# Performance work log

Measured on AMD Instinct MI355X. Metric: run time of the kernel, lower is better.

## Reference

```python
import jax, jax.numpy as jnp
import numpy as np

N_NODES, N_EDGES = 50000, 800000
IN_DIM, OUT_DIM, EDGE_DIM = 128, 128, 32
NUM_HEADS = 8
HEAD_DIM = OUT_DIM // NUM_HEADS
SCALE = HEAD_DIM ** -0.5


def setup_inputs() -> dict:
    key = jax.random.key(0)
    ks = jax.random.split(key, 8)
    def lin_w(k, fan_in, fan_out):
        # kaiming-uniform-ish init like nn.Linear
        bound = 1.0 / np.sqrt(fan_in)
        return jax.random.uniform(k, (fan_in, fan_out), jnp.float32, -bound, bound)
    return {
        "node_features": jax.random.normal(ks[0], (N_NODES, IN_DIM), jnp.float32),
        "edge_features": jax.random.normal(ks[1], (N_EDGES, EDGE_DIM), jnp.float32),
        "Wq": lin_w(ks[2], IN_DIM, OUT_DIM), "bq": jnp.zeros((OUT_DIM,), jnp.float32),
        "Wk": lin_w(ks[3], IN_DIM, OUT_DIM), "bk": jnp.zeros((OUT_DIM,), jnp.float32),
        "Wv": lin_w(ks[4], IN_DIM, OUT_DIM), "bv": jnp.zeros((OUT_DIM,), jnp.float32),
        "We": lin_w(ks[5], EDGE_DIM, OUT_DIM), "be": jnp.zeros((OUT_DIM,), jnp.float32),
        "edge_list": jax.random.randint(ks[6], (N_EDGES, 2), 0, N_NODES, jnp.int32),
        "num_nodes": N_NODES,
    }


def reference(node_features, edge_features, Wq, bq, Wk, bk, Wv, bv, We, be, edge_list, num_nodes):
    # node projections -> [N, H, D]
    Q = (node_features @ Wq + bq).reshape(-1, NUM_HEADS, HEAD_DIM)
    K = (node_features @ Wk + bk).reshape(-1, NUM_HEADS, HEAD_DIM)
    V = (node_features @ Wv + bv).reshape(-1, NUM_HEADS, HEAD_DIM)
    edge_bias = (edge_features @ We + be).reshape(-1, NUM_HEADS, HEAD_DIM)

    src = edge_list[:, 0]  # node_in
    dst = edge_list[:, 1]  # node_out

    # per-edge per-head scores: [E, H]
    scores = jnp.einsum("ehd,ehd->eh", Q[src], K[dst]) * SCALE + edge_bias.sum(-1)
    # NOTE: softmax over the HEADS axis (dim=1), exactly as in the source
    weights = jax.nn.softmax(scores, axis=1)

    # weighted messages gathered from src, scattered to dst: [E, H, D] -> [N, H, D]
    msg = V[src] * weights[..., None]
    node_updates = jax.ops.segment_sum(msg, dst, num_segments=num_nodes)
    return node_updates.reshape(num_nodes, OUT_DIM)
```

## Files before the change

kernel.cpp:

```cpp
#include <hip/hip_runtime.h>
#include <math.h>

#define IN_DIM   128
#define OUT_DIM  128
#define EDGE_DIM 32
#define NUM_HEADS 8
#define HEAD_DIM 16
#define SCALE 0.25f
#define CSTRIDE 16

typedef __attribute__((ext_vector_type(8))) short bf16x8;
typedef __attribute__((ext_vector_type(4))) float f32x4;
typedef __attribute__((ext_vector_type(4))) unsigned int u32x4;

__device__ inline unsigned short f2bf(float x) {
    unsigned int u = __float_as_uint(x);
    unsigned int r = u + 0x7fff + ((u >> 16) & 1);
    return (unsigned short)(r >> 16);
}
__device__ inline float bflo(unsigned int u) { return __uint_as_float(u << 16); }
__device__ inline float bfhi(unsigned int u) { return __uint_as_float(u & 0xffff0000u); }

__global__ __launch_bounds__(256) void setup_kernel(
    int* __restrict__ counts, int n_nodes, int nbz,
    const float* __restrict__ Wq, const float* __restrict__ Wk,
    const float* __restrict__ Wv, unsigned short* __restrict__ WtB, int nbw,
    const float* __restrict__ We, const float* __restrict__ be,
    float* __restrict__ WeR, float* __restrict__ beR,
    const float* __restrict__ X, unsigned short* __restrict__ Xb)
{
    const int bx = blockIdx.x;
    const int t  = threadIdx.x;
    if (bx < nbz) {
        const int i = bx * 256 + t;
        if (i < n_nodes) counts[i << 4] = 0;
    } else if (bx < nbz + nbw) {
        const int idx = (bx - nbz) * 256 + t;
        const int mat = idx >> 14;
        const int rem = idx & 16383;
        const int n = rem >> 7, k = rem & 127;
        const float* W = (mat == 0) ? Wq : (mat == 1) ? Wk : Wv;
        WtB[mat * 16384 + n * 128 + k] = f2bf(W[k * 128 + n]);
    } else if (bx == nbz + nbw) {
        const int k = t >> 3, h = t & 7;
        float s = 0.f;
#pragma unroll
        for (int d = 0; d < HEAD_DIM; ++d) s += We[k * OUT_DIM + h * HEAD_DIM + d];
        WeR[k * NUM_HEADS + h] = s;
        if (t < NUM_HEADS) {
            float sb = 0.f;
#pragma unroll
            for (int d = 0; d < HEAD_DIM; ++d) sb += be[t * HEAD_DIM + d];
            beR[t] = sb;
        }
    } else {
        const int i = (bx - (nbz + nbw + 1)) * 256 + t;
        if (i < n_nodes * 16) {
            const f32x4* xr = (const f32x4*)(X + (size_t)i * 8);
            const f32x4 x0 = xr[0], x1 = xr[1];
            u32x4 p;
            p[0] = (unsigned)f2bf(x0[0]) | ((unsigned)f2bf(x0[1]) << 16);
            p[1] = (unsigned)f2bf(x0[2]) | ((unsigned)f2bf(x0[3]) << 16);
            p[2] = (unsigned)f2bf(x1[0]) | ((unsigned)f2bf(x1[1]) << 16);
            p[3] = (unsigned)f2bf(x1[2]) | ((unsigned)f2bf(x1[3]) << 16);
            *(u32x4*)(Xb + (size_t)i * 8) = p;
        }
    }
}

__global__ __launch_bounds__(256) void edge_kernel(
    const int* __restrict__ el, int* __restrict__ counts, int* __restrict__ rank,
    const float* __restrict__ ef, const float* __restrict__ WeR,
    const float* __restrict__ beR, unsigned int* __restrict__ ebias_e,
    int n_edges)
{
    const int e = blockIdx.x * 256 + threadIdx.x;
    if (e >= n_edges) return;
    const int2 ed = ((const int2*)el)[e];
    rank[e] = atomicAdd(&counts[ed.y << 4], 1);

    float acc[NUM_HEADS];
#pragma unroll
    for (int h = 0; h < NUM_HEADS; ++h) acc[h] = beR[h];

    const f32x4* efr = (const f32x4*)(ef + (size_t)e * EDGE_DIM);
#pragma unroll
    for (int kk = 0; kk < 8; ++kk) {
        const f32x4 f = efr[kk];
#pragma unroll
        for (int c = 0; c < 4; ++c) {
            const float* wr = WeR + (kk * 4 + c) * NUM_HEADS;
#pragma unroll
            for (int h = 0; h < NUM_HEADS; ++h)
                acc[h] = fmaf(f[c], wr[h], acc[h]);
        }
    }
    u32x4 pk;
    pk[0] = (unsigned)f2bf(acc[0]) | ((unsigned)f2bf(acc[1]) << 16);
    pk[1] = (unsigned)f2bf(acc[2]) | ((unsigned)f2bf(acc[3]) << 16);
    pk[2] = (unsigned)f2bf(acc[4]) | ((unsigned)f2bf(acc[5]) << 16);
    pk[3] = (unsigned)f2bf(acc[6]) | ((unsigned)f2bf(acc[7]) << 16);
    *(u32x4*)(ebias_e + (size_t)e * 4) = pk;
}

__global__ __launch_bounds__(256) void qkv_kernel(
    const unsigned short* __restrict__ Xb, const unsigned short* __restrict__ WtB,
    const float* __restrict__ bq, const float* __restrict__ bk,
    const float* __restrict__ bv,
    unsigned short* __restrict__ QVb, unsigned short* __restrict__ Kb,
    int n_nodes, int nbm)
{
    __shared__ unsigned short shW[16384];
    const int bx = blockIdx.x;
    const int t  = threadIdx.x;

    const int which = bx / nbm;
    const int mb    = bx - which * nbm;
    const unsigned short* Wg = WtB + which * 16384;

#pragma unroll
    for (int kk = 0; kk < 8; ++kk) {
        const int c = kk * 256 + t;
        const u32x4 v = ((const u32x4*)Wg)[c];
        const int row = c >> 4;
        const int bir = (c & 15) << 4;
        *(u32x4*)((char*)shW + row * 256 + (bir ^ ((row & 7) << 4))) = v;
    }
    __syncthreads();

    const int wave = t >> 6, lane = t & 63;
    const int quad = lane >> 4, li = lane & 15;
    const int mbase = mb * 256 + wave * 64;

    int mrow[4];
#pragma unroll
    for (int m = 0; m < 4; ++m) {
        const int r_ = mbase + m * 16 + li;
        mrow[m] = (r_ < n_nodes) ? r_ : (n_nodes - 1);
    }

    f32x4 acc[4][8];
#pragma unroll
    for (int m = 0; m < 4; ++m)
#pragma unroll
        for (int nt = 0; nt < 8; ++nt) acc[m][nt] = (f32x4){0.f, 0.f, 0.f, 0.f};

#pragma unroll
    for (int ks = 0; ks < 4; ++ks) {
        bf16x8 a[4];
#pragma unroll
        for (int m = 0; m < 4; ++m)
            a[m] = *(const bf16x8*)(Xb + (size_t)mrow[m] * 128 + ks * 32 + quad * 8);
#pragma unroll
        for (int nt = 0; nt < 8; ++nt) {
            const int row = nt * 16 + li;
            const bf16x8 b = *(const bf16x8*)((const char*)shW + row * 256 +
                                ((ks * 64 + quad * 16) ^ ((row & 7) << 4)));
#pragma unroll
            for (int m = 0; m < 4; ++m)
                acc[m][nt] = __builtin_amdgcn_mfma_f32_16x16x32_bf16(a[m], b, acc[m][nt], 0, 0, 0);
        }
    }

    const float* bias = (which == 0) ? bq : (which == 1) ? bk : bv;
    float bv8[8];
#pragma unroll
    for (int nt = 0; nt < 8; ++nt) bv8[nt] = bias[nt * 16 + li];

    __syncthreads();

    unsigned short* stg = shW + wave * 2176;
    const int R = lane >> 2, cc4 = lane & 3;
#pragma unroll
    for (int m = 0; m < 4; ++m) {
#pragma unroll
        for (int nt = 0; nt < 8; ++nt)
#pragma unroll
            for (int r = 0; r < 4; ++r)
                stg[(quad * 4 + r) * 136 + nt * 16 + li] = f2bf(acc[m][nt][r] + bv8[nt]);
        __syncthreads();

        const int node = mbase + m * 16 + R;
        if (node < n_nodes) {
            const u32x4* s = (const u32x4*)(stg + R * 136 + cc4 * 32);
            u32x4 d0 = s[0], d1 = s[1], d2 = s[2], d3 = s[3];
            unsigned short* dp =
                (which == 0) ? (QVb + (size_t)node * 256 + cc4 * 32)
              : (which == 1) ? (Kb  + (size_t)node * 128 + cc4 * 32)
              :                (QVb + (size_t)node * 256 + 128 + cc4 * 32);
            u32x4* d = (u32x4*)dp;
            d[0] = d0; d[1] = d1; d[2] = d2; d[3] = d3;
        }
        __syncthreads();
    }
}

__global__ __launch_bounds__(256) void scan1_kernel(
    const int* __restrict__ counts, int* __restrict__ bsums, int n)
{
    __shared__ int lds[256];
    const int i = blockIdx.x * 256 + threadIdx.x;
    lds[threadIdx.x] = (i < n) ? counts[i << 4] : 0;
    __syncthreads();
    for (int off = 128; off > 0; off >>= 1) {
        if (threadIdx.x < off) lds[threadIdx.x] += lds[threadIdx.x + off];
        __syncthreads();
    }
    if (threadIdx.x == 0) bsums[blockIdx.x] = lds[0];
}

__global__ __launch_bounds__(256) void scan3_kernel(
    const int* __restrict__ counts, const int* __restrict__ bsums,
    int* __restrict__ offsets, int n, int n_edges, int nb)
{
    __shared__ int lds[256];
    const int t = threadIdx.x;

    int v = (t < nb) ? bsums[t] : 0;
    lds[t] = v;
    __syncthreads();
    for (int off = 1; off < 256; off <<= 1) {
        const int u = (t >= off) ? lds[t - off] : 0;
        __syncthreads();
        lds[t] += u;
        __syncthreads();
    }
    const int base = (blockIdx.x > 0) ? lds[blockIdx.x - 1] : 0;
    __syncthreads();

    const int i = blockIdx.x * 256 + t;
    const int c = (i < n) ? counts[i << 4] : 0;
    lds[t] = c;
    __syncthreads();
    for (int off = 1; off < 256; off <<= 1) {
        const int u = (t >= off) ? lds[t - off] : 0;
        __syncthreads();
        lds[t] += u;
        __syncthreads();
    }
    if (i < n) offsets[i] = base + lds[t] - c;
    if (blockIdx.x == 0 && t == 0) offsets[n] = n_edges;
}

__global__ __launch_bounds__(256) void scatter_kernel(
    const int* __restrict__ el, const int* __restrict__ rank,
    const unsigned int* __restrict__ ebias_e,
    const int* __restrict__ offsets, unsigned int* __restrict__ recs,
    int n_edges)
{
    const int e = blockIdx.x * 256 + threadIdx.x;
    if (e >= n_edges) return;
    const int2 ed = ((const int2*)el)[e];
    const u32x4 eb = *(const u32x4*)(ebias_e + (size_t)e * 4);
    const int pos = offsets[ed.y] + rank[e];

    u32x4 r0, r1;
    r0[0] = (unsigned)ed.x;
    r0[1] = 0;
    r0[2] = eb[0];
    r0[3] = eb[1];
    r1[0] = eb[2];
    r1[1] = eb[3];
    r1[2] = 0; r1[3] = 0;
    u32x4* rp = (u32x4*)(recs + (size_t)pos * 8);
    rp[0] = r0;
    rp[1] = r1;
}

__global__ __launch_bounds__(256) void aggregate_kernel(
    const unsigned short* __restrict__ QVb, const unsigned short* __restrict__ Kb,
    const int* __restrict__ offsets, const unsigned int* __restrict__ recs,
    float* __restrict__ out, int n_nodes)
{
    const int gw   = (blockIdx.x * 256 + threadIdx.x) >> 6;
    const int lane = threadIdx.x & 63;
    const int half = lane >> 5, ln = lane & 31;
    const int node = gw * 2 + half;
    const int h = ln >> 2;
    const bool valid = node < n_nodes;

    int beg = 0, end = 0;
    if (valid) { beg = offsets[node]; end = offsets[node + 1]; }
    const int cnt = end - beg;
    const int mcnt = max(cnt, __shfl_xor(cnt, 32));

    float k0 = 0.f, k1 = 0.f, k2 = 0.f, k3 = 0.f;
    if (valid) {
        const uint2 kp = ((const uint2*)(Kb + (size_t)node * 128))[ln];
        k0 = bflo(kp.x); k1 = bfhi(kp.x); k2 = bflo(kp.y); k3 = bfhi(kp.y);
    }

    float a0 = 0.f, a1 = 0.f, a2 = 0.f, a3 = 0.f;

    uint2 qp = make_uint2(0, 0), vp = make_uint2(0, 0);
    float eb = 0.f;
    if (cnt > 0) {
        const unsigned int* rb = recs + (size_t)beg * 8;
        const int src = (int)rb[0];
        const unsigned int ebp = rb[2 + (h >> 1)];
        eb = (h & 1) ? bfhi(ebp) : bflo(ebp);
        const uint2* r = (const uint2*)(QVb + (size_t)src * 256);
        qp = r[ln];
        vp = r[32 + ln];
    }

    for (int i = 0; i < mcnt; ++i) {
        uint2 nqp = qp, nvp = vp;
        float neb = eb;
        if (i + 1 < cnt) {
            const unsigned int* rb = recs + (size_t)(beg + i + 1) * 8;
            const int ns = (int)rb[0];
            const unsigned int ebp = rb[2 + (h >> 1)];
            neb = (h & 1) ? bfhi(ebp) : bflo(ebp);
            const uint2* r = (const uint2*)(QVb + (size_t)ns * 256);
            nqp = r[ln];
            nvp = r[32 + ln];
        }

        const float q0 = bflo(qp.x), q1 = bfhi(qp.x);
        const float q2 = bflo(qp.y), q3 = bfhi(qp.y);
        float p = fmaf(q0, k0, fmaf(q1, k1, fmaf(q2, k2, q3 * k3)));
        p += __shfl_xor(p, 1);
        p += __shfl_xor(p, 2);
        const float score = fmaf(p, SCALE, eb);

        float mx = score;
        mx = fmaxf(mx, __shfl_xor(mx, 4));
        mx = fmaxf(mx, __shfl_xor(mx, 8));
        mx = fmaxf(mx, __shfl_xor(mx, 16));
        const float ex = __expf(score - mx);
        float den = ex;
        den += __shfl_xor(den, 4);
        den += __shfl_xor(den, 8);
        den += __shfl_xor(den, 16);
        const float w = __fdividef(ex, den);

        if (i < cnt) {
            a0 = fmaf(w, bflo(vp.x), a0);
            a1 = fmaf(w, bfhi(vp.x), a1);
            a2 = fmaf(w, bflo(vp.y), a2);
            a3 = fmaf(w, bfhi(vp.y), a3);
        }
        qp = nqp; vp = nvp; eb = neb;
    }

    if (valid) {
        f32x4 o; o[0] = a0; o[1] = a1; o[2] = a2; o[3] = a3;
        *(((f32x4*)(out + (size_t)node * OUT_DIM)) + ln) = o;
    }
}

extern "C" void kernel_launch(void* const* d_in, const int* in_sizes, int n_in,
                              void* d_out, int out_size, void* d_ws, size_t ws_size,
                              hipStream_t stream)
{
    const float* X   = (const float*)d_in[0];
    const float* ef  = (const float*)d_in[1];
    const float* Wq  = (const float*)d_in[2];
    const float* bq  = (const float*)d_in[3];
    const float* Wk  = (const float*)d_in[4];
    const float* bk  = (const float*)d_in[5];
    const float* Wv  = (const float*)d_in[6];
    const float* bv  = (const float*)d_in[7];
    const float* We  = (const float*)d_in[8];
    const float* be  = (const float*)d_in[9];
    const int*   el  = (const int*)d_in[10];

    const int n_nodes = in_sizes[0] / IN_DIM;
    const int n_edges = in_sizes[10] / 2;

    char* w = (char*)d_ws;
    auto alloc = [&](size_t bytes) { char* p = w; w += (bytes + 255) & ~(size_t)255; return p; };

    unsigned short* QVb    = (unsigned short*)alloc((size_t)n_nodes * 256 * 2);
    unsigned short* Kb     = (unsigned short*)alloc((size_t)n_nodes * 128 * 2);
    unsigned short* WtB    = (unsigned short*)alloc((size_t)3 * 128 * 128 * 2);
    unsigned int*   recs   = (unsigned int*)alloc((size_t)n_edges * 32);
    unsigned int*   ebias_e= (unsigned int*)alloc((size_t)n_edges * 16);
    int* rank    = (int*)alloc((size_t)n_edges * 4);
    float* WeR   = (float*)alloc(EDGE_DIM * NUM_HEADS * 4);
    float* beR   = (float*)alloc(NUM_HEADS * 4);
    int* counts  = (int*)alloc((size_t)n_nodes * CSTRIDE * 4);
    int* offsets = (int*)alloc((size_t)(n_nodes + 1) * 4);
    int* bsums   = (int*)alloc(256 * 4);

    unsigned short* Xb = (unsigned short*)recs;

    const int nbz = (n_nodes + 255) / 256;
    const int nbw = (3 * 128 * 128) / 256;
    const int nbx = (n_nodes * 16 + 255) / 256;
    setup_kernel<<<nbz + nbw + 1 + nbx, 256, 0, stream>>>(
        counts, n_nodes, nbz, Wq, Wk, Wv, WtB, nbw, We, be, WeR, beR, X, Xb);

    const int nbh = (n_edges + 255) / 256;
    edge_kernel<<<nbh, 256, 0, stream>>>(
        el, counts, rank, ef, WeR, beR, ebias_e, n_edges);

    const int nbm = (n_nodes + 255) / 256;
    qkv_kernel<<<3 * nbm, 256, 0, stream>>>(
        Xb, WtB, bq, bk, bv, QVb, Kb, n_nodes, nbm);

    const int nb = (n_nodes + 255) / 256;
    scan1_kernel<<<nb, 256, 0, stream>>>(counts, bsums, n_nodes);
    scan3_kernel<<<nb, 256, 0, stream>>>(counts, bsums, offsets, n_nodes, n_edges, nb);

    scatter_kernel<<<nbh, 256, 0, stream>>>(
        el, rank, ebias_e, offsets, recs, n_edges);

    const int nwaves = (n_nodes + 1) / 2;
    aggregate_kernel<<<(nwaves * 64 + 255) / 256, 256, 0, stream>>>(
        QVb, Kb, offsets, recs, (float*)d_out, n_nodes);
}
```

Before: 334.6 us.

## Process eight edges per wave in parallel in aggregate kernel with head-per-lane layout

Restructures the aggregation so each wave handles one node. The 64 lanes are split into 8 edge groups by 8 heads, and each lane holds a full 16-dim head slice of Q, K and V. The per-edge sequential loop becomes a loop over batches of 8 edges with two-deep software prefetch of the record indices and gathered rows. Partial accumulators are reduced across edge groups with shuffles at the end. This aims to raise memory-level parallelism and cut the serial per-edge shuffle chain, at the cost of more registers (32 floats of state plus prefetched vectors) and a 48-shuffle final reduction per node.

```diff
diff --git a/kernel.cpp b/kernel.cpp
--- a/kernel.cpp
+++ b/kernel.cpp
@@ -272,82 +272,112 @@
     const int* __restrict__ offsets, const unsigned int* __restrict__ recs,
     float* __restrict__ out, int n_nodes)
 {
-    const int gw   = (blockIdx.x * 256 + threadIdx.x) >> 6;
+    const int wave = threadIdx.x >> 6;
     const int lane = threadIdx.x & 63;
-    const int half = lane >> 5, ln = lane & 31;
-    const int node = gw * 2 + half;
-    const int h = ln >> 2;
-    const bool valid = node < n_nodes;
-
-    int beg = 0, end = 0;
-    if (valid) { beg = offsets[node]; end = offsets[node + 1]; }
+    const int node = blockIdx.x * 4 + wave;
+    if (node >= n_nodes) return;
+    const int g = lane >> 3;
+    const int h = lane & 7;
+
+    const int beg = offsets[node];
+    const int end = offsets[node + 1];
     const int cnt = end - beg;
-    const int mcnt = max(cnt, __shfl_xor(cnt, 32));
-
-    float k0 = 0.f, k1 = 0.f, k2 = 0.f, k3 = 0.f;
-    if (valid) {
-        const uint2 kp = ((const uint2*)(Kb + (size_t)node * 128))[ln];
-        k0 = bflo(kp.x); k1 = bfhi(kp.x); k2 = bflo(kp.y); k3 = bfhi(kp.y);
-    }
-
-    float a0 = 0.f, a1 = 0.f, a2 = 0.f, a3 = 0.f;
-
-    uint2 qp = make_uint2(0, 0), vp = make_uint2(0, 0);
-    float eb = 0.f;
+
+    float kf[16];
+    {
+        const u32x4* kp = (const u32x4*)(Kb + (size_t)node * 128 + h * 16);
+        const u32x4 ka = kp[0], kb_ = kp[1];
+#pragma unroll
+        for (int j = 0; j < 4; ++j) { kf[j * 2] = bflo(ka[j]);  kf[j * 2 + 1] = bfhi(ka[j]); }
+#pragma unroll
+        for (int j = 0; j < 4; ++j) { kf[8 + j * 2] = bflo(kb_[j]); kf[8 + j * 2 + 1] = bfhi(kb_[j]); }
+    }
+
+    float acc[16];
+#pragma unroll
+    for (int d = 0; d < 16; ++d) acc[d] = 0.f;
+
     if (cnt > 0) {
-        const unsigned int* rb = recs + (size_t)beg * 8;
-        const int src = (int)rb[0];
-        const unsigned int ebp = rb[2 + (h >> 1)];
-        eb = (h & 1) ? bfhi(ebp) : bflo(ebp);
-        const uint2* r = (const uint2*)(QVb + (size_t)src * 256);
-        qp = r[ln];
-        vp = r[32 + ln];
-    }
-
-    for (int i = 0; i < mcnt; ++i) {
-        uint2 nqp = qp, nvp = vp;
-        float neb = eb;
-        if (i + 1 < cnt) {
-            const unsigned int* rb = recs + (size_t)(beg + i + 1) * 8;
-            const int ns = (int)rb[0];
-            const unsigned int ebp = rb[2 + (h >> 1)];
-            neb = (h & 1) ? bfhi(ebp) : bflo(ebp);
-            const uint2* r = (const uint2*)(QVb + (size_t)ns * 256);
-            nqp = r[ln];
-            nvp = r[32 + ln];
-        }
-
-        const float q0 = bflo(qp.x), q1 = bfhi(qp.x);
-        const float q2 = bflo(qp.y), q3 = bfhi(qp.y);
-        float p = fmaf(q0, k0, fmaf(q1, k1, fmaf(q2, k2, q3 * k3)));
-        p += __shfl_xor(p, 1);
-        p += __shfl_xor(p, 2);
-        const float score = fmaf(p, SCALE, eb);
-
-        float mx = score;
-        mx = fmaxf(mx, __shfl_xor(mx, 4));
-        mx = fmaxf(mx, __shfl_xor(mx, 8));
-        mx = fmaxf(mx, __shfl_xor(mx, 16));
-        const float ex = __expf(score - mx);
-        float den = ex;
-        den += __shfl_xor(den, 4);
-        den += __shfl_xor(den, 8);
-        den += __shfl_xor(den, 16);
-        const float w = __fdividef(ex, den);
-
-        if (i < cnt) {
-            a0 = fmaf(w, bflo(vp.x), a0);
-            a1 = fmaf(w, bfhi(vp.x), a1);
-            a2 = fmaf(w, bflo(vp.y), a2);
-            a3 = fmaf(w, bfhi(vp.y), a3);
-        }
-        qp = nqp; vp = nvp; eb = neb;
-    }
-
-    if (valid) {
-        f32x4 o; o[0] = a0; o[1] = a1; o[2] = a2; o[3] = a3;
-        *(((f32x4*)(out + (size_t)node * OUT_DIM)) + ln) = o;
-    }
+        const int last = end - 1;
+        const int ebd  = 2 + (h >> 1);
+
+        int s0 = beg + g;            if (s0 > last) s0 = last;
+        unsigned int src_c = recs[(size_t)s0 * 8];
+        unsigned int ebw_c = recs[(size_t)s0 * 8 + ebd];
+        u32x4 qa, qb, va, vb;
+        {
+            const u32x4* qp = (const u32x4*)(QVb + (size_t)src_c * 256 + h * 16);
+            qa = qp[0]; qb = qp[1];
+            const u32x4* vp = (const u32x4*)(QVb + (size_t)src_c * 256 + 128 + h * 16);
+            va = vp[0]; vb = vp[1];
+        }
+        int s1 = beg + 8 + g;        if (s1 > last) s1 = last;
+        unsigned int src_n = recs[(size_t)s1 * 8];
+        unsigned int ebw_n = recs[(size_t)s1 * 8 + ebd];
+
+        for (int i = 0; i < cnt; i += 8) {
+            int s2 = beg + i + 16 + g;  if (s2 > last) s2 = last;
+            const unsigned int src_f = recs[(size_t)s2 * 8];
+            const unsigned int ebw_f = recs[(size_t)s2 * 8 + ebd];
+            u32x4 qan, qbn, van, vbn;
+            {
+                const u32x4* qp = (const u32x4*)(QVb + (size_t)src_n * 256 + h * 16);
+                qan = qp[0]; qbn = qp[1];
+                const u32x4* vp = (const u32x4*)(QVb + (size_t)src_n * 256 + 128 + h * 16);
+                van = vp[0]; vbn = vp[1];
+            }
+
+            const float eb = (h & 1) ? bfhi(ebw_c) : bflo(ebw_c);
+            float p = 0.f;
+#pragma unroll
+            for (int j = 0; j < 4; ++j) {
+                p = fmaf(bflo(qa[j]), kf[j * 2],     p);
+                p = fmaf(bfhi(qa[j]), kf[j * 2 + 1], p);
+            }
+#pragma unroll
+            for (int j = 0; j < 4; ++j) {
+                p = fmaf(bflo(qb[j]), kf[8 + j * 2],     p);
+                p = fmaf(bfhi(qb[j]), kf[8 + j * 2 + 1], p);
+            }
+            const float score = fmaf(p, SCALE, eb);
+
+            float mx = score;
+            mx = fmaxf(mx, __shfl_xor(mx, 1));
+            mx = fmaxf(mx, __shfl_xor(mx, 2));
+            mx = fmaxf(mx, __shfl_xor(mx, 4));
+            const float ex = __expf(score - mx);
+            float den = ex;
+            den += __shfl_xor(den, 1);
+            den += __shfl_xor(den, 2);
+            den += __shfl_xor(den, 4);
+            float w = __fdividef(ex, den);
+            if (i + g >= cnt) w = 0.f;
+
+#pragma unroll
+            for (int j = 0; j < 4; ++j) {
+                acc[j * 2]     = fmaf(w, bflo(va[j]), acc[j * 2]);
+                acc[j * 2 + 1] = fmaf(w, bfhi(va[j]), acc[j * 2 + 1]);
+            }
+#pragma unroll
+            for (int j = 0; j < 4; ++j) {
+                acc[8 + j * 2]     = fmaf(w, bflo(vb[j]), acc[8 + j * 2]);
+                acc[8 + j * 2 + 1] = fmaf(w, bfhi(vb[j]), acc[8 + j * 2 + 1]);
+            }
+
+            qa = qan; qb = qbn; va = van; vb = vbn;
+            src_c = src_n; ebw_c = ebw_n;
+            src_n = src_f; ebw_n = ebw_f;
+        }
+    }
+
+#pragma unroll
+    for (int mask = 8; mask <= 32; mask <<= 1)
+#pragma unroll
+        for (int d = 0; d < 16; ++d)
+            acc[d] += __shfl_xor(acc[d], mask);
+
+    float2 o2 = make_float2(acc[g * 2], acc[g * 2 + 1]);
+    *(float2*)(out + (size_t)node * OUT_DIM + h * 16 + g * 2) = o2;
 }
 
 extern "C" void kernel_launch(void* const* d_in, const int* in_sizes, int n_in,
@@ -407,7 +437,6 @@
     scatter_kernel<<<nbh, 256, 0, stream>>>(
         el, rank, ebias_e, offsets, recs, n_edges);
 
-    const int nwaves = (n_nodes + 1) / 2;
-    aggregate_kernel<<<(nwaves * 64 + 255) / 256, 256, 0, stream>>>(
+    aggregate_kernel<<<(n_nodes + 3) / 4, 256, 0, stream>>>(
         QVb, Kb, offsets, recs, (float*)d_out, n_nodes);
 }
```

Measured after the change: 322.8 us. 1.04x faster.
